# Kernel tuning notes

Measured on AMD Instinct MI355X. Metric: run time of the kernel, lower is better.

## Reference

```python
import jax, jax.numpy as jnp
import numpy as np

N_NODES = 50000
N_EDGES = 800000
N_GRAPHS = 100
IN_DIM = 100
OUT_DIM = 128
N_ETYPES = 4
N_STEPS = 8


def setup_inputs() -> dict:
    key = jax.random.key(0)
    ks = jax.random.split(key, 16)
    s = 0.05
    return {
        "features": jax.random.normal(ks[0], (N_NODES, IN_DIM), jnp.float32),
        "edge_src": jax.random.randint(ks[1], (N_EDGES,), 0, N_NODES, jnp.int32),
        "edge_dst": jax.random.randint(ks[2], (N_EDGES,), 0, N_NODES, jnp.int32),
        "edge_types": jax.random.randint(ks[3], (N_EDGES,), 0, N_ETYPES, jnp.int32),
        "graph_ids": jnp.sort(jax.random.randint(ks[4], (N_NODES,), 0, N_GRAPHS, jnp.int32)),
        "W_msg": jax.random.normal(ks[5], (N_ETYPES, OUT_DIM, OUT_DIM), jnp.float32) * s,
        "b_msg": jax.random.normal(ks[6], (N_ETYPES, OUT_DIM), jnp.float32) * s,
        "W_ih": jax.random.normal(ks[7], (3 * OUT_DIM, OUT_DIM), jnp.float32) * s,
        "W_hh": jax.random.normal(ks[8], (3 * OUT_DIM, OUT_DIM), jnp.float32) * s,
        "b_ih": jax.random.normal(ks[9], (3 * OUT_DIM,), jnp.float32) * s,
        "b_hh": jax.random.normal(ks[10], (3 * OUT_DIM,), jnp.float32) * s,
        "W1": jax.random.normal(ks[11], (256, OUT_DIM), jnp.float32) * s,
        "b1": jax.random.normal(ks[12], (256,), jnp.float32) * s,
        "W2": jax.random.normal(ks[13], (1, 256), jnp.float32) * s,
        "b2": jax.random.normal(ks[14], (1,), jnp.float32) * s,
    }


def _gru_cell(x, h, W_ih, W_hh, b_ih, b_hh):
    # torch.nn.GRUCell: gate order (reset, update, new)
    gi = x @ W_ih.T + b_ih  # [N, 3D]
    gh = h @ W_hh.T + b_hh
    i_r, i_z, i_n = jnp.split(gi, 3, axis=-1)
    h_r, h_z, h_n = jnp.split(gh, 3, axis=-1)
    r = jax.nn.sigmoid(i_r + h_r)
    z = jax.nn.sigmoid(i_z + h_z)
    n = jnp.tanh(i_n + r * h_n)
    return (1.0 - z) * n + z * h


def reference(features, edge_src, edge_dst, edge_types, graph_ids,
              W_msg, b_msg, W_ih, W_hh, b_ih, b_hh, W1, b1, W2, b2):
    n_nodes = features.shape[0]
    # DGL GatedGraphConv: zero-pad input features to out_feats
    h = jnp.pad(features, ((0, 0), (0, OUT_DIM - features.shape[1])))
    for _ in range(N_STEPS):
        # per-edge-type linear transform of source features: [T, N, D]
        transformed = jnp.einsum('nd,tdf->tnf', h, W_msg) + b_msg[:, None, :]
        msgs = transformed[edge_types, edge_src]  # [E, D] gather
        a = jax.ops.segment_sum(msgs, edge_dst, num_segments=n_nodes)  # scatter-add
        h = _gru_cell(a, h, W_ih, W_hh, b_ih, b_hh)
    # masked mean pooling per graph (mask_mean over de-batchified graphs)
    counts = jax.ops.segment_sum(jnp.ones((n_nodes,), h.dtype), graph_ids,
                                 num_segments=N_GRAPHS)
    sums = jax.ops.segment_sum(h, graph_ids, num_segments=N_GRAPHS)
    pooled = sums / jnp.maximum(counts, 1.0)[:, None]  # [B, D]
    # classifier: Linear -> relu -> (dropout: eval noop) -> Linear -> sigmoid
    hidden = jax.nn.relu(pooled @ W1.T + b1)
    logits = hidden @ W2.T + b2  # [B, 1]
    return jax.nn.sigmoid(logits).squeeze(-1)  # [B]
```

## Files before the change

kernel.cpp:

```cpp
#include <hip/hip_runtime.h>
#include <hip/hip_bf16.h>
#include <math.h>

#define N_NODES 50000
#define M_PAD   50048
#define N_EDGES 800000
#define N_GRAPHS 100
#define IN_DIM 100
#define D 128
#define N_STEPS 8
#define NBINS (N_NODES * 4)
#define SCAN_BLOCKS 196

typedef unsigned short ushort_t;
typedef __bf16 bf16x8 __attribute__((ext_vector_type(8)));
typedef float f32x4 __attribute__((ext_vector_type(4)));

__device__ inline ushort_t f2b(float f) {
  __hip_bfloat16 b = __float2bfloat16(f);
  return *reinterpret_cast<ushort_t*>(&b);
}
__device__ inline float b2f(unsigned int u16) {
  unsigned int x = u16 << 16;
  return __builtin_bit_cast(float, x);
}

__device__ __attribute__((always_inline)) inline void gld16(const ushort_t* g, ushort_t* l) {
  __builtin_amdgcn_global_load_lds(
      (const __attribute__((address_space(1))) void*)g,
      (__attribute__((address_space(3))) void*)l, 16, 0, 0);
}

__global__ void pad_cast_kernel(const float* __restrict__ feat, ushort_t* __restrict__ ah) {
  int idx = blockIdx.x * blockDim.x + threadIdx.x;
  if (idx >= N_NODES * D) return;
  int n = idx >> 7, d = idx & 127;
  float v = (d < IN_DIM) ? feat[n * IN_DIM + d] : 0.0f;
  ah[(size_t)n * 256 + 128 + d] = f2b(v);
}

__global__ void prep_bts(const float* __restrict__ W_msg, ushort_t* __restrict__ BtS) {
  int idx = blockIdx.x * blockDim.x + threadIdx.x;
  if (idx >= 128 * 512) return;
  int f = idx >> 9, kp = idx & 511;
  int t = kp >> 7, k = kp & 127;
  BtS[(size_t)f * 512 + kp] = f2b(W_msg[((size_t)t * 128 + k) * 128 + f]);
}

__global__ void prep_wg(const float* __restrict__ W_ih, const float* __restrict__ W_hh,
                        const float* __restrict__ b_ih, const float* __restrict__ b_hh,
                        ushort_t* __restrict__ WgT, float* __restrict__ gbias) {
  int idx = blockIdx.x * blockDim.x + threadIdx.x;
  if (idx >= 512 * 256) return;
  int colp = idx >> 8, k = idx & 255;
  int g = colp >> 6, gate = (colp >> 4) & 3, r = colp & 15;
  int d = g * 16 + r;
  float v;
  if (gate == 3)      v = (k < 128) ? 0.f : W_hh[(size_t)(256 + d) * 128 + (k - 128)];
  else if (gate == 2) v = (k < 128) ? W_ih[(size_t)(256 + d) * 128 + k] : 0.f;
  else {
    int j0 = (gate == 0) ? d : 128 + d;
    v = (k < 128) ? W_ih[(size_t)j0 * 128 + k] : W_hh[(size_t)j0 * 128 + (k - 128)];
  }
  WgT[(size_t)colp * 256 + k] = f2b(v);
  if (k == 0) {
    float bb = (gate == 0) ? b_ih[d] + b_hh[d]
             : (gate == 1) ? b_ih[128 + d] + b_hh[128 + d]
             : (gate == 2) ? b_ih[256 + d] : b_hh[256 + d];
    gbias[colp] = bb;
  }
}

__global__ void hist_kernel(const int* __restrict__ edst, const int* __restrict__ etype,
                            int* __restrict__ cnt2, int* __restrict__ rank) {
  int e = blockIdx.x * 256 + threadIdx.x;
  if (e >= N_EDGES) return;
  rank[e] = atomicAdd(&cnt2[edst[e] * 4 + etype[e]], 1);
}

__global__ __launch_bounds__(1024) void scanA(const int* __restrict__ cnt2,
                                              int* __restrict__ tmp, int* __restrict__ bsum) {
  __shared__ int wsum[16];
  int b = blockIdx.x, t = threadIdx.x;
  int i = b * 1024 + t;
  int lane = t & 63, wid = t >> 6;
  int x = (i < NBINS) ? cnt2[i] : 0;
  #pragma unroll
  for (int s = 1; s < 64; s <<= 1) {
    int y = __shfl_up(x, s, 64);
    if (lane >= s) x += y;
  }
  if (lane == 63) wsum[wid] = x;
  __syncthreads();
  if (wid == 0) {
    int w = (lane < 16) ? wsum[lane] : 0;
    #pragma unroll
    for (int s = 1; s < 16; s <<= 1) {
      int y = __shfl_up(w, s, 64);
      if (lane >= s) w += y;
    }
    if (lane < 16) wsum[lane] = w;
  }
  __syncthreads();
  int wb = (wid > 0) ? wsum[wid - 1] : 0;
  tmp[i] = wb + x;
  if (t == 1023) bsum[b] = wsum[15];
}

__global__ __launch_bounds__(64) void scanB(const int* __restrict__ bsum,
                                            int* __restrict__ bpre) {
  int lane = threadIdx.x;
  int carry = 0;
  for (int base = 0; base < SCAN_BLOCKS; base += 64) {
    int idx = base + lane;
    int v = (idx < SCAN_BLOCKS) ? bsum[idx] : 0;
    int x = v;
    #pragma unroll
    for (int s = 1; s < 64; s <<= 1) {
      int y = __shfl_up(x, s, 64);
      if (lane >= s) x += y;
    }
    if (idx < SCAN_BLOCKS) bpre[idx] = carry + x - v;
    carry += __shfl(x, 63, 64);
  }
}

__global__ __launch_bounds__(1024) void scanC(const int* __restrict__ tmp,
                                              const int* __restrict__ bpre,
                                              int* __restrict__ offs2) {
  int b = blockIdx.x, t = threadIdx.x;
  int i = b * 1024 + t;
  if (i < NBINS) offs2[i + 1] = tmp[i] + bpre[b];
  if (i == 0) offs2[0] = 0;
}

__global__ void fill_kernel(const int* __restrict__ esrc, const int* __restrict__ edst,
                            const int* __restrict__ etype, const int* __restrict__ offs2,
                            const int* __restrict__ rank, int* __restrict__ payload) {
  int e = blockIdx.x * 256 + threadIdx.x;
  if (e >= N_EDGES) return;
  int key = edst[e] * 4 + etype[e];
  payload[offs2[key] + rank[e]] = esrc[e];
}

__global__ __launch_bounds__(256) void gather_kernel(const int* __restrict__ offs2,
    const int* __restrict__ payload, const ushort_t* __restrict__ hb,
    ushort_t* __restrict__ S, float* __restrict__ cntf) {
  int n = blockIdx.x * 4 + (threadIdx.x >> 6);
  int lane = threadIdx.x & 63;
  if (n >= N_NODES) return;
  int bb[5];
  #pragma unroll
  for (int k = 0; k < 5; ++k) bb[k] = offs2[n * 4 + k];
  float a[4][2] = {{0.f, 0.f}, {0.f, 0.f}, {0.f, 0.f}, {0.f, 0.f}};
  const ushort_t* hrow = hb + 128 + lane * 2;
  for (int base = bb[0]; base < bb[4]; base += 64) {
    int lim = min(bb[4], base + 64);
    int cnt = lim - base;
    int pe = (lane < cnt) ? payload[base + lane] : 0;
    #pragma unroll
    for (int t = 0; t < 4; ++t) {
      int lo = max(bb[t], base), hi = min(bb[t + 1], lim);
      int i = lo;
      for (; i + 4 <= hi; i += 4) {
        int s0 = __shfl(pe, i - base, 64);
        int s1 = __shfl(pe, i + 1 - base, 64);
        int s2 = __shfl(pe, i + 2 - base, 64);
        int s3 = __shfl(pe, i + 3 - base, 64);
        unsigned int u0 = *(const unsigned int*)(hrow + (size_t)s0 * 256);
        unsigned int u1 = *(const unsigned int*)(hrow + (size_t)s1 * 256);
        unsigned int u2 = *(const unsigned int*)(hrow + (size_t)s2 * 256);
        unsigned int u3 = *(const unsigned int*)(hrow + (size_t)s3 * 256);
        a[t][0] += b2f(u0 & 0xffff) + b2f(u1 & 0xffff) + b2f(u2 & 0xffff) + b2f(u3 & 0xffff);
        a[t][1] += b2f(u0 >> 16) + b2f(u1 >> 16) + b2f(u2 >> 16) + b2f(u3 >> 16);
      }
      for (; i < hi; ++i) {
        int s0 = __shfl(pe, i - base, 64);
        unsigned int u0 = *(const unsigned int*)(hrow + (size_t)s0 * 256);
        a[t][0] += b2f(u0 & 0xffff);
        a[t][1] += b2f(u0 >> 16);
      }
    }
  }
  #pragma unroll
  for (int t = 0; t < 4; ++t) {
    unsigned int packed = (unsigned int)f2b(a[t][0]) | ((unsigned int)f2b(a[t][1]) << 16);
    *(unsigned int*)(S + (size_t)n * 512 + t * 128 + lane * 2) = packed;
    if (lane == 0) cntf[n * 4 + t] = (float)(bb[t + 1] - bb[t]);
  }
}

template <int MODE>
__global__ __launch_bounds__(256) void mfma_gemm(
    const ushort_t* __restrict__ A, int lda, int K,
    const ushort_t* __restrict__ Bt,
    const float* __restrict__ bias, const float* __restrict__ b_msg,
    const float* __restrict__ cntf,
    ushort_t* __restrict__ ah_out) {
  __shared__ __align__(16) unsigned char smem[15360];
  ushort_t* As = (ushort_t*)smem;
  ushort_t* Bs = (ushort_t*)(smem + 4096);
  const int m0 = blockIdx.x * 64, n0 = blockIdx.y * 128;
  int tid = threadIdx.x;
  int wave = tid >> 6, lane = tid & 63;
  int wm = (wave & 1) * 32, wn = (wave >> 1) * 64;
  int quad = lane >> 4, l16 = lane & 15;

  int sr = lane >> 2, sc = lane & 3;
  const ushort_t* gA  = A  + (size_t)(m0 + wave * 16 + sr) * lda + sc * 8;
  const ushort_t* gB0 = Bt + (size_t)(n0 + wave * 32 + sr) * K   + sc * 8;
  const ushort_t* gB1 = gB0 + (size_t)16 * K;
  ushort_t* lA  = As + wave * 512;
  ushort_t* lB0 = Bs + wave * 1024;
  ushort_t* lB1 = Bs + wave * 1024 + 512;

  f32x4 acc[2][4];
  #pragma unroll
  for (int i = 0; i < 2; ++i)
    #pragma unroll
    for (int j = 0; j < 4; ++j) acc[i][j] = (f32x4){0.f, 0.f, 0.f, 0.f};

  for (int k0 = 0; k0 < K; k0 += 32) {
    gld16(gA + k0, lA);
    gld16(gB0 + k0, lB0);
    gld16(gB1 + k0, lB1);
    __syncthreads();
    bf16x8 af[2], bfr[4];
    #pragma unroll
    for (int i = 0; i < 2; ++i) af[i] = *(const bf16x8*)&As[(wm + i * 16 + l16) * 32 + quad * 8];
    #pragma unroll
    for (int j = 0; j < 4; ++j) bfr[j] = *(const bf16x8*)&Bs[(wn + j * 16 + l16) * 32 + quad * 8];
    #pragma unroll
    for (int i = 0; i < 2; ++i)
      #pragma unroll
      for (int j = 0; j < 4; ++j)
        acc[i][j] = __builtin_amdgcn_mfma_f32_16x16x32_bf16(af[i], bfr[j], acc[i][j], 0, 0, 0);
    __syncthreads();
  }

  if (MODE == 2) {
    ushort_t* Ep = (ushort_t*)smem;
    float bm[4][4];
    #pragma unroll
    for (int j = 0; j < 4; ++j)
      #pragma unroll
      for (int t = 0; t < 4; ++t)
        bm[j][t] = b_msg[t * 128 + wn + j * 16 + l16];
    #pragma unroll
    for (int p = 0; p < 2; ++p) {
      if (p) __syncthreads();
      #pragma unroll
      for (int reg = 0; reg < 4; ++reg) {
        int slot = (wm >> 5) * 16 + quad * 4 + reg;
        int m = m0 + wm + p * 16 + quad * 4 + reg;
        float4 c = *(const float4*)(cntf + (size_t)m * 4);
        #pragma unroll
        for (int j = 0; j < 4; ++j) {
          float val = acc[p][j][reg] + c.x * bm[j][0] + c.y * bm[j][1]
                                     + c.z * bm[j][2] + c.w * bm[j][3];
          Ep[slot * 136 + wn + j * 16 + l16] = f2b(val);
        }
      }
      __syncthreads();
      #pragma unroll
      for (int c2 = 0; c2 < 2; ++c2) {
        int chunk = tid + 256 * c2;
        int slot = chunk >> 4, sub = chunk & 15;
        int m = m0 + (slot & 15) + (slot >> 4) * 32 + p * 16;
        *(uint4*)(ah_out + (size_t)m * 256 + sub * 8) =
            *(const uint4*)&Ep[slot * 136 + sub * 8];
      }
    }
  } else {
    ushort_t* Ap = (ushort_t*)smem;
    int db = (n0 >> 6) * 16;
    int dim_loc = (wn >> 6) * 16 + l16;
    float br = bias[n0 + wn + l16];
    float bz = bias[n0 + wn + 16 + l16];
    float bi = bias[n0 + wn + 32 + l16];
    float bh = bias[n0 + wn + 48 + l16];
    #pragma unroll
    for (int i = 0; i < 2; ++i)
      #pragma unroll
      for (int reg = 0; reg < 4; ++reg) {
        int r_loc = wm + i * 16 + quad * 4 + reg;
        int m = m0 + r_loc;
        float pr  = acc[i][0][reg] + br;
        float pz  = acc[i][1][reg] + bz;
        float in_ = acc[i][2][reg] + bi;
        float hn  = acc[i][3][reg] + bh;
        float r = 1.0f / (1.0f + expf(-pr));
        float z = 1.0f / (1.0f + expf(-pz));
        float nn = tanhf(in_ + r * hn);
        float hold = b2f(A[(size_t)m * lda + 128 + db + dim_loc]);
        float hv = (1.0f - z) * nn + z * hold;
        Ap[r_loc * 40 + dim_loc] = f2b(hv);
      }
    __syncthreads();
    {
      int row = tid >> 2, sub = tid & 3;
      *(uint4*)(ah_out + (size_t)(m0 + row) * 256 + 128 + db + sub * 8) =
          *(const uint4*)&Ap[row * 40 + sub * 8];
    }
  }
}

__global__ __launch_bounds__(128) void pool_kernel(const ushort_t* __restrict__ ah,
    const int* __restrict__ gids, float* __restrict__ pooled, float* __restrict__ gcnt) {
  __shared__ int lo_s, hi_s;
  int g = blockIdx.x, c = blockIdx.y, d = threadIdx.x;
  if (d == 0) {
    int lo = 0, hi = N_NODES;
    while (lo < hi) { int mid = (lo + hi) >> 1; if (gids[mid] < g) lo = mid + 1; else hi = mid; }
    lo_s = lo;
    int lo2 = lo, hi2 = N_NODES;
    while (lo2 < hi2) { int mid = (lo2 + hi2) >> 1; if (gids[mid] < g + 1) lo2 = mid + 1; else hi2 = mid; }
    hi_s = lo2;
  }
  __syncthreads();
  int lo = lo_s, hi = hi_s;
  int len = hi - lo;
  int b = lo + (int)(((long long)len * c) >> 3);
  int e = lo + (int)(((long long)len * (c + 1)) >> 3);
  float s = 0.f;
  for (int n = b; n < e; ++n) s += b2f(ah[(size_t)n * 256 + 128 + d]);
  if (e > b) atomicAdd(&pooled[g * 128 + d], s);
  if (c == 0 && d == 0) gcnt[g] = (float)len;
}

__global__ __launch_bounds__(256) void classifier_kernel(
    const float* __restrict__ pooled, const float* __restrict__ gcnt,
    const float* __restrict__ W1, const float* __restrict__ b1,
    const float* __restrict__ W2, const float* __restrict__ b2,
    float* __restrict__ out) {
  __shared__ float p[D];
  __shared__ float hid[256];
  __shared__ float wsum[4];
  int g = blockIdx.x;
  int t = threadIdx.x;
  float cnt = fmaxf(gcnt[g], 1.0f);
  if (t < D) p[t] = pooled[g * D + t] / cnt;
  __syncthreads();
  float acc = b1[t];
  const float* w = W1 + (size_t)t * D;
  for (int k = 0; k < D; ++k) acc += p[k] * w[k];
  hid[t] = fmaxf(acc, 0.0f);
  __syncthreads();
  float v = hid[t] * W2[t];
  for (int off = 32; off > 0; off >>= 1) v += __shfl_down(v, off, 64);
  if ((t & 63) == 0) wsum[t >> 6] = v;
  __syncthreads();
  if (t == 0) {
    float s = wsum[0] + wsum[1] + wsum[2] + wsum[3] + b2[0];
    out[g] = 1.0f / (1.0f + expf(-s));
  }
}

extern "C" void kernel_launch(void* const* d_in, const int* in_sizes, int n_in,
                              void* d_out, int out_size, void* d_ws, size_t ws_size,
                              hipStream_t stream) {
  const float* features = (const float*)d_in[0];
  const int* esrc  = (const int*)d_in[1];
  const int* edst  = (const int*)d_in[2];
  const int* etype = (const int*)d_in[3];
  const int* gids  = (const int*)d_in[4];
  const float* W_msg = (const float*)d_in[5];
  const float* b_msg = (const float*)d_in[6];
  const float* W_ih  = (const float*)d_in[7];
  const float* W_hh  = (const float*)d_in[8];
  const float* b_ih  = (const float*)d_in[9];
  const float* b_hh  = (const float*)d_in[10];
  const float* W1 = (const float*)d_in[11];
  const float* b1 = (const float*)d_in[12];
  const float* W2 = (const float*)d_in[13];
  const float* b2 = (const float*)d_in[14];
  float* out = (float*)d_out;

  char* ws = (char*)d_ws;
  size_t off_b = 0;
  auto alloc = [&](size_t bytes) -> void* {
    void* p = ws + off_b;
    off_b += (bytes + 255) & ~(size_t)255;
    return p;
  };
  ushort_t* ahA    = (ushort_t*)alloc((size_t)M_PAD * 256 * 2);
  ushort_t* ahB    = (ushort_t*)alloc((size_t)M_PAD * 256 * 2);
  ushort_t* S      = (ushort_t*)alloc((size_t)M_PAD * 512 * 2);
  float*    cntf   = (float*)alloc((size_t)M_PAD * 4 * 4);
  ushort_t* BtS    = (ushort_t*)alloc(128 * 512 * 2);
  ushort_t* WgT    = (ushort_t*)alloc(512 * 256 * 2);
  float*    gbias  = (float*)alloc(512 * 4);
  int*      cnt2   = (int*)alloc((size_t)NBINS * 4);
  int*      offs2  = (int*)alloc((size_t)(NBINS + 1) * 4);
  int*      rank   = (int*)alloc((size_t)N_EDGES * 4);
  int*      tmp    = (int*)alloc((size_t)SCAN_BLOCKS * 1024 * 4);
  int*      bsum   = (int*)alloc(SCAN_BLOCKS * 4);
  int*      bpre   = (int*)alloc(SCAN_BLOCKS * 4);
  int*      payload= (int*)alloc((size_t)N_EDGES * 4);
  float*    pooled = (float*)alloc(N_GRAPHS * 128 * 4);
  float*    gcnt   = (float*)alloc(N_GRAPHS * 4);

  pad_cast_kernel<<<(N_NODES * 128 + 255) / 256, 256, 0, stream>>>(features, ahA);
  prep_bts<<<(128 * 512 + 255) / 256, 256, 0, stream>>>(W_msg, BtS);
  prep_wg<<<(512 * 256 + 255) / 256, 256, 0, stream>>>(W_ih, W_hh, b_ih, b_hh, WgT, gbias);
  hipMemsetAsync(cnt2, 0, (size_t)NBINS * 4, stream);
  hist_kernel<<<(N_EDGES + 255) / 256, 256, 0, stream>>>(edst, etype, cnt2, rank);
  scanA<<<SCAN_BLOCKS, 1024, 0, stream>>>(cnt2, tmp, bsum);
  scanB<<<1, 64, 0, stream>>>(bsum, bpre);
  scanC<<<SCAN_BLOCKS, 1024, 0, stream>>>(tmp, bpre, offs2);
  fill_kernel<<<(N_EDGES + 255) / 256, 256, 0, stream>>>(esrc, edst, etype, offs2, rank, payload);

  ushort_t* cur = ahA;
  ushort_t* nxt = ahB;
  for (int step = 0; step < N_STEPS; ++step) {
    gather_kernel<<<(N_NODES + 3) / 4, 256, 0, stream>>>(offs2, payload, cur, S, cntf);
    mfma_gemm<2><<<dim3(M_PAD / 64, 1), 256, 0, stream>>>(
        S, 512, 512, BtS, nullptr, b_msg, cntf, cur);
    mfma_gemm<1><<<dim3(M_PAD / 64, 4), 256, 0, stream>>>(
        cur, 256, 256, WgT, gbias, nullptr, nullptr, nxt);
    ushort_t* t2 = cur; cur = nxt; nxt = t2;
  }

  hipMemsetAsync(pooled, 0, (size_t)N_GRAPHS * 128 * 4, stream);
  pool_kernel<<<dim3(N_GRAPHS, 8), 128, 0, stream>>>(cur, gids, pooled, gcnt);
  classifier_kernel<<<N_GRAPHS, 256, 0, stream>>>(pooled, gcnt, W1, b1, W2, b2, out);
}
```

Measured before the change: 954.8 us.

## Multi-buffer MFMA GEMM K-loop with async prefetch and explicit waitcnt

```diff
diff --git a/kernel.cpp b/kernel.cpp
--- a/kernel.cpp
+++ b/kernel.cpp
@@ -190,16 +190,17 @@
   }
 }
 
-template <int MODE>
+template <int MODE, int K>
 __global__ __launch_bounds__(256) void mfma_gemm(
-    const ushort_t* __restrict__ A, int lda, int K,
+    const ushort_t* __restrict__ A, int lda,
     const ushort_t* __restrict__ Bt,
     const float* __restrict__ bias, const float* __restrict__ b_msg,
     const float* __restrict__ cntf,
     ushort_t* __restrict__ ah_out) {
-  __shared__ __align__(16) unsigned char smem[15360];
-  ushort_t* As = (ushort_t*)smem;
-  ushort_t* Bs = (ushort_t*)(smem + 4096);
+  constexpr int NT  = K / 32;
+  constexpr int PRE = 3;
+  constexpr int SLOT = 12288;
+  __shared__ __align__(16) unsigned char smem[SLOT * 4];
   const int m0 = blockIdx.x * 64, n0 = blockIdx.y * 128;
   int tid = threadIdx.x;
   int wave = tid >> 6, lane = tid & 63;
@@ -210,9 +211,14 @@
   const ushort_t* gA  = A  + (size_t)(m0 + wave * 16 + sr) * lda + sc * 8;
   const ushort_t* gB0 = Bt + (size_t)(n0 + wave * 32 + sr) * K   + sc * 8;
   const ushort_t* gB1 = gB0 + (size_t)16 * K;
-  ushort_t* lA  = As + wave * 512;
-  ushort_t* lB0 = Bs + wave * 1024;
-  ushort_t* lB1 = Bs + wave * 1024 + 512;
+
+  auto stage = [&](int slot, int t) {
+    ushort_t* base = (ushort_t*)(smem + slot * SLOT);
+    int k0 = t * 32;
+    gld16(gA + k0,  base + wave * 512);
+    gld16(gB0 + k0, base + 2048 + wave * 1024);
+    gld16(gB1 + k0, base + 2048 + wave * 1024 + 512);
+  };
 
   f32x4 acc[2][4];
   #pragma unroll
@@ -220,11 +226,19 @@
     #pragma unroll
     for (int j = 0; j < 4; ++j) acc[i][j] = (f32x4){0.f, 0.f, 0.f, 0.f};
 
-  for (int k0 = 0; k0 < K; k0 += 32) {
-    gld16(gA + k0, lA);
-    gld16(gB0 + k0, lB0);
-    gld16(gB1 + k0, lB1);
-    __syncthreads();
+  #pragma unroll
+  for (int t = 0; t < PRE; ++t) stage(t, t);
+
+  #pragma unroll
+  for (int t = 0; t < NT; ++t) {
+    int infl = NT - 1 - t;
+    if (infl >= 2)      asm volatile("s_waitcnt vmcnt(6) lgkmcnt(0)" ::: "memory");
+    else if (infl == 1) asm volatile("s_waitcnt vmcnt(3) lgkmcnt(0)" ::: "memory");
+    else                asm volatile("s_waitcnt vmcnt(0) lgkmcnt(0)" ::: "memory");
+    __builtin_amdgcn_s_barrier();
+    if (t + PRE < NT) stage((t + PRE) & 3, t + PRE);
+    const ushort_t* As = (const ushort_t*)(smem + (t & 3) * SLOT);
+    const ushort_t* Bs = As + 2048;
     bf16x8 af[2], bfr[4];
     #pragma unroll
     for (int i = 0; i < 2; ++i) af[i] = *(const bf16x8*)&As[(wm + i * 16 + l16) * 32 + quad * 8];
@@ -235,7 +249,6 @@
       #pragma unroll
       for (int j = 0; j < 4; ++j)
         acc[i][j] = __builtin_amdgcn_mfma_f32_16x16x32_bf16(af[i], bfr[j], acc[i][j], 0, 0, 0);
-    __syncthreads();
   }
 
   if (MODE == 2) {
@@ -414,10 +427,10 @@
   ushort_t* nxt = ahB;
   for (int step = 0; step < N_STEPS; ++step) {
     gather_kernel<<<(N_NODES + 3) / 4, 256, 0, stream>>>(offs2, payload, cur, S, cntf);
-    mfma_gemm<2><<<dim3(M_PAD / 64, 1), 256, 0, stream>>>(
-        S, 512, 512, BtS, nullptr, b_msg, cntf, cur);
-    mfma_gemm<1><<<dim3(M_PAD / 64, 4), 256, 0, stream>>>(
-        cur, 256, 256, WgT, gbias, nullptr, nullptr, nxt);
+    mfma_gemm<2, 512><<<dim3(M_PAD / 64, 1), 256, 0, stream>>>(
+        S, 512, BtS, nullptr, b_msg, cntf, cur);
+    mfma_gemm<1, 256><<<dim3(M_PAD / 64, 4), 256, 0, stream>>>(
+        cur, 256, WgT, gbias, nullptr, nullptr, nxt);
     ushort_t* t2 = cur; cur = nxt; nxt = t2;
   }
 
```

Measured after the change: 924.0 us. -3.2%, faster.
